# Kernel optimization log

Hardware: AMD Instinct MI355X
Metric: run time of the kernel (lower is better)

The kernel has to match this reference:

```python
import jax, jax.numpy as jnp
import numpy as np

FEA, ATT, HLAST, STEP = 256, 64, 10, 12
H = FEA * HLAST  # lstm hidden/cell size = 2560
IN = 2 * H       # concat(input, hidden) = 5120


def setup_inputs() -> dict:
    key = jax.random.key(0)
    ks = jax.random.split(key, 16)
    s = lambda k, shp, fan: jax.random.normal(k, shp, jnp.float32) * (1.0 / np.sqrt(fan))
    return {
        "x": jax.random.normal(ks[0], (64 * STEP, FEA, ATT), jnp.float32),
        # encoder: Linear(64->128), Linear(128->10) (stored as [in,out])
        "W0": s(ks[1], (ATT, 128), ATT), "b0": jnp.zeros((128,), jnp.float32),
        "W1": s(ks[2], (128, HLAST), 128), "b1": jnp.zeros((HLAST,), jnp.float32),
        # LSTM gates: forget, input, output, cell  [IN, H]
        "Wf": s(ks[3], (IN, H), IN), "bf": jnp.zeros((H,), jnp.float32),
        "Wi": s(ks[4], (IN, H), IN), "bi": jnp.zeros((H,), jnp.float32),
        "Wo": s(ks[5], (IN, H), IN), "bo": jnp.zeros((H,), jnp.float32),
        "Wc": s(ks[6], (IN, H), IN), "bc": jnp.zeros((H,), jnp.float32),
        # final fc: Linear(10->10)
        "Wfc": s(ks[7], (HLAST, HLAST), HLAST), "bfc": jnp.zeros((HLAST,), jnp.float32),
    }


def reference(x, W0, b0, W1, b1, Wf, bf, Wi, bi, Wo, bo, Wc, bc, Wfc, bfc):
    # encoder (dropout is identity at eval): Linear -> ReLU, twice
    h = x.reshape(-1, FEA, ATT)
    h = jax.nn.relu(h @ W0 + b0)            # [B*T, FEA, 128]
    h = jax.nn.relu(h @ W1 + b1)            # [B*T, FEA, 10]
    h = h.reshape(-1, STEP, H)              # [B, T, H]
    B = h.shape[0]

    def step_fn(carry, xt):
        hs, cs = carry                       # [B, H] each
        comb = jnp.concatenate([xt, hs], axis=1)  # [B, 2H]
        f = jax.nn.sigmoid(comb @ Wf + bf)
        i = jax.nn.sigmoid(comb @ Wi + bi)
        o = jax.nn.sigmoid(comb @ Wo + bo)
        g = jnp.tanh(comb @ Wc + bc)
        cs = f * cs + i * g
        hs = o * jnp.tanh(cs)
        return (hs, cs), None

    init = (jnp.zeros((B, H), h.dtype), jnp.zeros((B, H), h.dtype))
    (hs, _), _ = jax.lax.scan(step_fn, init, jnp.swapaxes(h, 0, 1))  # scan over time

    out = hs.reshape(B, FEA, HLAST)          # [B, 256, 10]
    out = jax.nn.relu(out) @ Wfc + bfc       # fc(ReLU(x))
    return out
```

## Files before the change

kernel.cpp:

```cpp
#include <hip/hip_runtime.h>
#include <math.h>

#define FEA   256
#define ATT   64
#define HLAST 10
#define NSTEP 12
#define HDIM  2560
#define BATCH 64
#define BT    768
#define KT_FULL 160
#define KT_HALF 80
#define NT_G  160
#define MT_E  48

typedef _Float16 h8_t __attribute__((ext_vector_type(8)));
typedef float    f4_t __attribute__((ext_vector_type(4)));

__device__ __forceinline__ float sigm(float x) { return 1.0f / (1.0f + expf(-x)); }

__global__ __launch_bounds__(256) void k_pack_enc(
    const float* __restrict__ W0, const float* __restrict__ W1,
    _Float16* __restrict__ Bp0, _Float16* __restrict__ Bp1)
{
  const int tid = threadIdx.x;
  for (int e = tid; e < 16 * 512; e += 256) {
    const int frag = e >> 9, idx = e & 511, l = idx >> 3, j = idx & 7;
    const int nt = frag >> 1, kt = frag & 1;
    const int k = kt * 32 + (l >> 4) * 8 + j;
    const int n = nt * 16 + (l & 15);
    Bp0[e] = (_Float16)W0[k * 128 + n];
  }
  for (int e = tid; e < 4 * 512; e += 256) {
    const int kt = e >> 9, idx = e & 511, l = idx >> 3, j = idx & 7;
    const int k = kt * 32 + (l >> 4) * 8 + j;
    const int n = l & 15;
    Bp1[e] = (n < HLAST) ? (_Float16)W1[k * HLAST + n] : (_Float16)0.0f;
  }
}

__global__ __launch_bounds__(256) void k_enc_conv(
    const float* __restrict__ x, const _Float16* __restrict__ Bp0,
    const _Float16* __restrict__ Bp1, const float* __restrict__ b0,
    const float* __restrict__ b1, _Float16* __restrict__ Ep,
    const float* __restrict__ Wf, const float* __restrict__ Wi,
    const float* __restrict__ Wo, const float* __restrict__ Wc,
    _Float16* __restrict__ Wp)
{
  __shared__ __align__(16) _Float16 sA[4][16][136];
  const int grp = blockIdx.x / 37, r37 = blockIdx.x % 37;
  const int tid = threadIdx.x;

  if (r37 >= 12) {
    float (*tile)[130] = (float(*)[130])(void*)sA;
    const int cid = grp * 25 + (r37 - 12);
    const int g = cid / 1600;
    const int r = cid % 1600;
    const int kt = r / 20, cb = r % 20;
    const float* __restrict__ W = (g == 0) ? Wf : (g == 1) ? Wi : (g == 2) ? Wo : Wc;
    const float* src = W + (size_t)(kt * 32) * HDIM + cb * 128;
    #pragma unroll
    for (int s = 0; s < 4; ++s) {
      const int slot = s * 256 + tid;
      const int rr = slot >> 5, c4 = slot & 31;
      float4 v = *(const float4*)&src[(size_t)rr * HDIM + c4 * 4];
      *(float4*)&tile[rr][c4 * 4] = v;
    }
    __syncthreads();
    const int l = tid & 63, w = tid >> 6;
    const int k0 = (l >> 4) * 8, c16 = l & 15;
    #pragma unroll
    for (int s = 0; s < 2; ++s) {
      const int f = w * 2 + s;
      h8_t h;
      #pragma unroll
      for (int j = 0; j < 8; ++j) h[j] = (_Float16)tile[k0 + j][f * 16 + c16];
      const int nt = cb * 8 + f;
      *(h8_t*)&Wp[(((size_t)(g * NT_G + nt) * KT_FULL + kt) << 9) + l * 8] = h;
    }
    return;
  }

  const int eid = grp * 12 + r37;
  const int l = tid & 63, w = tid >> 6;
  const int bt = eid >> 2;
  const int f0 = (eid & 3) * 64 + w * 16;
  const int rl = l >> 4, cl = l & 15;

  h8_t B0[16];
  #pragma unroll
  for (int q = 0; q < 16; ++q)
    B0[q] = *(const h8_t*)(Bp0 + (q << 9) + l * 8);

  const float* xr = x + ((size_t)bt * FEA + f0 + cl) * ATT + rl * 8;
  h8_t a0, a1;
  {
    float4 v0 = *(const float4*)(xr);
    float4 v1 = *(const float4*)(xr + 4);
    float4 v2 = *(const float4*)(xr + 32);
    float4 v3 = *(const float4*)(xr + 36);
    #pragma unroll
    for (int j = 0; j < 4; ++j) {
      a0[j]     = (_Float16)((const float*)&v0)[j];
      a0[4 + j] = (_Float16)((const float*)&v1)[j];
      a1[j]     = (_Float16)((const float*)&v2)[j];
      a1[4 + j] = (_Float16)((const float*)&v3)[j];
    }
  }
  f4_t acc1[8] = {};
  #pragma unroll
  for (int j = 0; j < 8; ++j) {
    acc1[j] = __builtin_amdgcn_mfma_f32_16x16x32_f16(a0, B0[j * 2 + 0], acc1[j], 0, 0, 0);
    acc1[j] = __builtin_amdgcn_mfma_f32_16x16x32_f16(a1, B0[j * 2 + 1], acc1[j], 0, 0, 0);
  }
  #pragma unroll
  for (int j = 0; j < 8; ++j) {
    const float bj = b0[j * 16 + cl];
    #pragma unroll
    for (int r = 0; r < 4; ++r)
      sA[w][rl * 4 + r][j * 16 + cl] = (_Float16)fmaxf(acc1[j][r] + bj, 0.0f);
  }
  f4_t acc2 = {};
  #pragma unroll
  for (int kt = 0; kt < 4; ++kt) {
    const h8_t a = *(const h8_t*)&sA[w][cl][kt * 32 + rl * 8];
    const h8_t b = *(const h8_t*)(Bp1 + (kt << 9) + l * 8);
    acc2 = __builtin_amdgcn_mfma_f32_16x16x32_f16(a, b, acc2, 0, 0, 0);
  }
  if (cl < HLAST) {
    const float b1v = b1[cl];
    #pragma unroll
    for (int r = 0; r < 4; ++r) {
      const int f = f0 + rl * 4 + r;
      const float val = fmaxf(acc2[r] + b1v, 0.0f);
      const int kf = f * HLAST + cl;
      const int mt = bt >> 4, kt2 = kf >> 5, gp = (kf >> 3) & 3, jj = kf & 7;
      Ep[(((size_t)mt * KT_HALF + kt2) << 9) + (((bt & 15) + 16 * gp) << 3) + jj] =
          (_Float16)val;
    }
  }
}

__global__ __launch_bounds__(512) void k_xpre_conv(
    const _Float16* __restrict__ Ep, _Float16* __restrict__ Wp,
    const float* __restrict__ bf, const float* __restrict__ bi,
    const float* __restrict__ bo, const float* __restrict__ bc,
    _Float16* __restrict__ Xpre,
    const float* __restrict__ Wf, const float* __restrict__ Wi,
    const float* __restrict__ Wo, const float* __restrict__ Wc)
{
  __shared__ __align__(16) _Float16 sB[2][16 * 512];
  const int bid = blockIdx.x, tid = threadIdx.x;

  if (bid % 21 != 0) {
    float (*tile)[130] = (float(*)[130])(void*)sB;
    const int cid = bid - bid / 21 - 1;
    const int g = cid / 1600;
    const int r = cid % 1600;
    const int kt = 80 + r / 20, cb = r % 20;
    const float* __restrict__ W = (g == 0) ? Wf : (g == 1) ? Wi : (g == 2) ? Wo : Wc;
    const float* src = W + (size_t)(kt * 32) * HDIM + cb * 128;
    #pragma unroll
    for (int s = 0; s < 2; ++s) {
      const int slot = s * 512 + tid;
      const int rr = slot >> 5, c4 = slot & 31;
      float4 v = *(const float4*)&src[(size_t)rr * HDIM + c4 * 4];
      *(float4*)&tile[rr][c4 * 4] = v;
    }
    __syncthreads();
    const int l = tid & 63, f = tid >> 6;
    const int k0 = (l >> 4) * 8, c16 = l & 15;
    h8_t h;
    #pragma unroll
    for (int j = 0; j < 8; ++j) h[j] = (_Float16)tile[k0 + j][f * 16 + c16];
    const int nt = cb * 8 + f;
    *(h8_t*)&Wp[(((size_t)(g * NT_G + nt) * KT_FULL + kt) << 9) + l * 8] = h;
    return;
  }

  const int rid = bid / 21;
  const int bx = rid % 40, by = (rid / 40) & 1, bz = rid / 80;
  const int g = bz, mh = by;
  const float* __restrict__ bias = (g == 0) ? bf : (g == 1) ? bi : (g == 2) ? bo : bc;
  const int nt0 = bx * 4;
  const int l = tid & 63, w = tid >> 6;
  const int mt0 = mh * 24 + w * 3;
  const _Float16* Bsrc = Wp + ((size_t)(g * NT_G + nt0) * KT_FULL) * 512 + l * 8;
  const _Float16* Asrc = Ep + ((size_t)mt0 * KT_HALF) * 512 + l * 8;

  f4_t acc[3][4] = {};

#define STAGE_XPRE(cc, buf)                                                       \
  {                                                                               \
    _Pragma("unroll")                                                             \
    for (int s = 0; s < 2; ++s) {                                                 \
      const int fi = s * 8 + w;                                                   \
      const int jj = fi >> 2, tt = fi & 3;                                        \
      const _Float16* gsrc = Bsrc + ((size_t)jj * KT_FULL + (cc) * 4 + tt) * 512; \
      __builtin_amdgcn_global_load_lds(                                           \
          (const __attribute__((address_space(1))) unsigned int*)(const void*)gsrc, \
          (__attribute__((address_space(3))) unsigned int*)(void*)&sB[buf][fi * 512], \
          16, 0, 0);                                                              \
    }                                                                             \
  }

  STAGE_XPRE(0, 0);
  __syncthreads();
  for (int cc = 0; cc < 20; ++cc) {
    const int buf = cc & 1;
    if (cc < 19) STAGE_XPRE(cc + 1, buf ^ 1);
    #pragma unroll
    for (int t = 0; t < 4; ++t) {
      const int kt = cc * 4 + t;
      h8_t b[4], a[3];
      #pragma unroll
      for (int j = 0; j < 4; ++j)
        b[j] = *(const h8_t*)&sB[buf][(j * 4 + t) * 512 + l * 8];
      #pragma unroll
      for (int i = 0; i < 3; ++i)
        a[i] = *(const h8_t*)(Asrc + ((size_t)i * KT_HALF + kt) * 512);
      #pragma unroll
      for (int i = 0; i < 3; ++i)
        #pragma unroll
        for (int j = 0; j < 4; ++j)
          acc[i][j] = __builtin_amdgcn_mfma_f32_16x16x32_f16(a[i], b[j], acc[i][j], 0, 0, 0);
    }
    __syncthreads();
  }

  const int rl = l >> 4, cl = l & 15;
  const int bn = nt0 * 16;
  #pragma unroll
  for (int j = 0; j < 4; ++j) {
    const int n = bn + j * 16 + cl;
    const float bv = bias[n];
    #pragma unroll
    for (int i = 0; i < 3; ++i)
      #pragma unroll
      for (int r = 0; r < 4; ++r) {
        const int m = (mt0 + i) * 16 + rl * 4 + r;
        Xpre[((size_t)g * BT + m) * HDIM + n] = (_Float16)(acc[i][j][r] + bv);
      }
  }
#undef STAGE_XPRE
}

__global__ __launch_bounds__(512) void k_step(
    const _Float16* __restrict__ hP, const _Float16* __restrict__ Wp,
    const _Float16* __restrict__ Xpre, float* __restrict__ cbuf,
    float* __restrict__ hbuf, _Float16* __restrict__ hPn, int tstep)
{
  __shared__ float pre_lds[8][32 * 17];
  const int tid = threadIdx.x, l = tid & 63, w = tid >> 6;
  const int g = w >> 1, kc = w & 1;
  const int nt = blockIdx.x, mh = blockIdx.y;
  const int kt0 = kc * 40;
  const int dir = tstep & 1;
  const int base = dir ? (kt0 + 39) : kt0;
  const int sgn = dir ? -1 : 1;

  const int ub = tid >> 4, un = tid & 15;
  const int brow = mh * 32 + ub;
  const int unf = nt * 16 + un;
  const size_t xr = ((size_t)brow * NSTEP + tstep) * HDIM + unf;
  const float xf = (float)Xpre[xr];
  const float xi = (float)Xpre[(size_t)1 * BT * HDIM + xr];
  const float xo = (float)Xpre[(size_t)2 * BT * HDIM + xr];
  const float xc = (float)Xpre[(size_t)3 * BT * HDIM + xr];
  const size_t ci = (size_t)brow * HDIM + unf;
  const float cold = cbuf[ci];

  const _Float16* Ab = hP + (((size_t)mh * 2 * KT_HALF) << 9) + l * 8;
  const _Float16* Bb = Wp + (((size_t)(g * NT_G + nt) * KT_FULL + KT_HALF) << 9) + l * 8;

  f4_t acc[2] = {};
  h8_t bq[12];
  #pragma unroll
  for (int s = 0; s < 12; ++s)
    bq[s] = *(const h8_t*)(Bb + ((size_t)(base + sgn * s) << 9));
  h8_t aq[4][2];
  #pragma unroll
  for (int s = 0; s < 4; ++s)
    #pragma unroll
    for (int i = 0; i < 2; ++i)
      aq[s][i] = *(const h8_t*)(Ab + (((size_t)(i * KT_HALF + base + sgn * s)) << 9));

  #pragma unroll
  for (int it = 0; it < 40; ++it) {
    const int kt = base + sgn * it;
    const h8_t bcur = bq[it % 12];
    const h8_t a0 = aq[it & 3][0], a1 = aq[it & 3][1];
    if (it < 28)
      bq[it % 12] = *(const h8_t*)(Bb + ((size_t)(kt + sgn * 12) << 9));
    if (it < 36) {
      aq[it & 3][0] = *(const h8_t*)(Ab + (((size_t)(0 * KT_HALF + kt + sgn * 4)) << 9));
      aq[it & 3][1] = *(const h8_t*)(Ab + (((size_t)(1 * KT_HALF + kt + sgn * 4)) << 9));
    }
    acc[0] = __builtin_amdgcn_mfma_f32_16x16x32_f16(a0, bcur, acc[0], 0, 0, 0);
    acc[1] = __builtin_amdgcn_mfma_f32_16x16x32_f16(a1, bcur, acc[1], 0, 0, 0);
  }

  float* pl = pre_lds[w];
  const int rl = l >> 4, cl = l & 15;
  #pragma unroll
  for (int i = 0; i < 2; ++i)
    #pragma unroll
    for (int r = 0; r < 4; ++r)
      pl[(i * 16 + rl * 4 + r) * 17 + cl] = acc[i][r];
  __syncthreads();
  {
    const int off = ub * 17 + un;
    float pf = xf, pi_ = xi, po = xo, pc = xc;
    #pragma unroll
    for (int kc2 = 0; kc2 < 2; ++kc2) {
      pf  += pre_lds[0 * 2 + kc2][off];
      pi_ += pre_lds[1 * 2 + kc2][off];
      po  += pre_lds[2 * 2 + kc2][off];
      pc  += pre_lds[3 * 2 + kc2][off];
    }
    const float f = sigm(pf), i_ = sigm(pi_), o = sigm(po), gg = tanhf(pc);
    const float cn = f * cold + i_ * gg;
    cbuf[ci] = cn;
    const float hn = o * tanhf(cn);
    if (tstep == NSTEP - 1) hbuf[ci] = hn;
    const int mt = brow >> 4, kt2 = unf >> 5, gp = (unf >> 3) & 3, j = unf & 7;
    hPn[(((size_t)mt * KT_HALF + kt2) << 9) + ((brow & 15) + 16 * gp) * 8 + j] = (_Float16)hn;
  }
}

__global__ __launch_bounds__(256) void k_out(
    const float* __restrict__ h, const float* __restrict__ Wfc,
    const float* __restrict__ bfc, float* __restrict__ out)
{
  __shared__ float sW[HLAST * HLAST], sb[HLAST];
  const int t = threadIdx.x;
  if (t < HLAST * HLAST) sW[t] = Wfc[t];
  if (t < HLAST) sb[t] = bfc[t];
  __syncthreads();
  const int idx = blockIdx.x * 256 + t;
  const int j = idx % HLAST;
  const int bf_ = idx / HLAST;
  float a = sb[j];
  #pragma unroll
  for (int k = 0; k < HLAST; ++k)
    a = fmaf(fmaxf(h[(size_t)bf_ * HLAST + k], 0.0f), sW[k * HLAST + j], a);
  out[idx] = a;
}

extern "C" void kernel_launch(void* const* d_in, const int* in_sizes, int n_in,
                              void* d_out, int out_size, void* d_ws, size_t ws_size,
                              hipStream_t stream)
{
  const float* x   = (const float*)d_in[0];
  const float* W0  = (const float*)d_in[1];
  const float* b0  = (const float*)d_in[2];
  const float* W1  = (const float*)d_in[3];
  const float* b1  = (const float*)d_in[4];
  const float* Wf  = (const float*)d_in[5];
  const float* bfp = (const float*)d_in[6];
  const float* Wi  = (const float*)d_in[7];
  const float* bip = (const float*)d_in[8];
  const float* Wo  = (const float*)d_in[9];
  const float* bop = (const float*)d_in[10];
  const float* Wc  = (const float*)d_in[11];
  const float* bcp = (const float*)d_in[12];
  const float* Wfc = (const float*)d_in[13];
  const float* bfc = (const float*)d_in[14];

  char* ws = (char*)d_ws;
  _Float16* Wp = (_Float16*)ws;                       ws += (size_t)4 * NT_G * KT_FULL * 512 * 2;
  _Float16* Ep = (_Float16*)ws;                       ws += (size_t)MT_E * KT_HALF * 512 * 2;
  _Float16* Xpre = (_Float16*)ws;                     ws += (size_t)4 * BT * HDIM * 2;
  float* cbuf  = (float*)ws;                          ws += (size_t)BATCH * HDIM * 4;
  float* hbuf  = (float*)ws;                          ws += (size_t)BATCH * HDIM * 4;
  _Float16* hPa = (_Float16*)ws;                      ws += (size_t)BATCH * HDIM * 2;
  _Float16* hPb = (_Float16*)ws;                      ws += (size_t)BATCH * HDIM * 2;
  _Float16* Bp0 = (_Float16*)ws;                      ws += (size_t)16 * 512 * 2;
  _Float16* Bp1 = (_Float16*)ws;                      ws += (size_t)4 * 512 * 2;

  hipMemsetAsync(cbuf, 0, (size_t)BATCH * HDIM * 4, stream);
  hipMemsetAsync(hPa, 0, (size_t)BATCH * HDIM * 2, stream);

  k_pack_enc<<<1, 256, 0, stream>>>(W0, W1, Bp0, Bp1);
  k_enc_conv<<<37 * 256, 256, 0, stream>>>(x, Bp0, Bp1, b0, b1, Ep,
                                           Wf, Wi, Wo, Wc, Wp);
  k_xpre_conv<<<21 * 320, 512, 0, stream>>>(Ep, Wp, bfp, bip, bop, bcp, Xpre,
                                            Wf, Wi, Wo, Wc);
  _Float16* hin = hPa;
  _Float16* hout = hPb;
  for (int t = 0; t < NSTEP; ++t) {
    k_step<<<dim3(NT_G, 2), 512, 0, stream>>>(hin, Wp, Xpre, cbuf, hbuf, hout, t);
    _Float16* tmp = hin; hin = hout; hout = tmp;
  }
  k_out<<<(BATCH * FEA * HLAST) / 256, 256, 0, stream>>>(hbuf, Wfc, bfc, (float*)d_out);
}
```

Measured before the change: 377.9 us.

## Merge batch halves into one block per column tile in LSTM step kernel

Each step-kernel block now covers all 64 batch rows instead of 32, so each loaded recurrent weight fragment feeds four MFMAs instead of two. This halves the reads of the large packed gate weights per step, at the cost of halving the grid to 160 blocks and doubling accumulator and LDS usage per block. The A-operand prefetch depth drops from 4 to 2 stages to keep register pressure in check.

```diff
diff --git a/kernel.cpp b/kernel.cpp
--- a/kernel.cpp
+++ b/kernel.cpp
@@ -249,81 +249,93 @@
     const _Float16* __restrict__ Xpre, float* __restrict__ cbuf,
     float* __restrict__ hbuf, _Float16* __restrict__ hPn, int tstep)
 {
-  __shared__ float pre_lds[8][32 * 17];
+  __shared__ float pre_lds[8][64 * 17];
   const int tid = threadIdx.x, l = tid & 63, w = tid >> 6;
   const int g = w >> 1, kc = w & 1;
-  const int nt = blockIdx.x, mh = blockIdx.y;
+  const int nt = blockIdx.x;
   const int kt0 = kc * 40;
   const int dir = tstep & 1;
   const int base = dir ? (kt0 + 39) : kt0;
   const int sgn = dir ? -1 : 1;
 
   const int ub = tid >> 4, un = tid & 15;
-  const int brow = mh * 32 + ub;
   const int unf = nt * 16 + un;
-  const size_t xr = ((size_t)brow * NSTEP + tstep) * HDIM + unf;
-  const float xf = (float)Xpre[xr];
-  const float xi = (float)Xpre[(size_t)1 * BT * HDIM + xr];
-  const float xo = (float)Xpre[(size_t)2 * BT * HDIM + xr];
-  const float xc = (float)Xpre[(size_t)3 * BT * HDIM + xr];
-  const size_t ci = (size_t)brow * HDIM + unf;
-  const float cold = cbuf[ci];
-
-  const _Float16* Ab = hP + (((size_t)mh * 2 * KT_HALF) << 9) + l * 8;
+  float xg0[4], xg1[4], cold0, cold1;
+  size_t ci0, ci1;
+  {
+    const size_t xr0 = ((size_t)ub * NSTEP + tstep) * HDIM + unf;
+    const size_t xr1 = ((size_t)(ub + 32) * NSTEP + tstep) * HDIM + unf;
+    #pragma unroll
+    for (int gg = 0; gg < 4; ++gg) {
+      xg0[gg] = (float)Xpre[(size_t)gg * BT * HDIM + xr0];
+      xg1[gg] = (float)Xpre[(size_t)gg * BT * HDIM + xr1];
+    }
+    ci0 = (size_t)ub * HDIM + unf;
+    ci1 = (size_t)(ub + 32) * HDIM + unf;
+    cold0 = cbuf[ci0];
+    cold1 = cbuf[ci1];
+  }
+
+  const _Float16* Ab = hP + l * 8;
   const _Float16* Bb = Wp + (((size_t)(g * NT_G + nt) * KT_FULL + KT_HALF) << 9) + l * 8;
 
-  f4_t acc[2] = {};
+  f4_t acc[4] = {};
   h8_t bq[12];
   #pragma unroll
   for (int s = 0; s < 12; ++s)
     bq[s] = *(const h8_t*)(Bb + ((size_t)(base + sgn * s) << 9));
-  h8_t aq[4][2];
-  #pragma unroll
-  for (int s = 0; s < 4; ++s)
-    #pragma unroll
-    for (int i = 0; i < 2; ++i)
+  h8_t aq[2][4];
+  #pragma unroll
+  for (int s = 0; s < 2; ++s)
+    #pragma unroll
+    for (int i = 0; i < 4; ++i)
       aq[s][i] = *(const h8_t*)(Ab + (((size_t)(i * KT_HALF + base + sgn * s)) << 9));
 
   #pragma unroll
   for (int it = 0; it < 40; ++it) {
     const int kt = base + sgn * it;
     const h8_t bcur = bq[it % 12];
-    const h8_t a0 = aq[it & 3][0], a1 = aq[it & 3][1];
+    const h8_t a0 = aq[it & 1][0], a1 = aq[it & 1][1];
+    const h8_t a2 = aq[it & 1][2], a3 = aq[it & 1][3];
     if (it < 28)
       bq[it % 12] = *(const h8_t*)(Bb + ((size_t)(kt + sgn * 12) << 9));
-    if (it < 36) {
-      aq[it & 3][0] = *(const h8_t*)(Ab + (((size_t)(0 * KT_HALF + kt + sgn * 4)) << 9));
-      aq[it & 3][1] = *(const h8_t*)(Ab + (((size_t)(1 * KT_HALF + kt + sgn * 4)) << 9));
+    if (it < 38) {
+      #pragma unroll
+      for (int i = 0; i < 4; ++i)
+        aq[it & 1][i] = *(const h8_t*)(Ab + (((size_t)(i * KT_HALF + kt + sgn * 2)) << 9));
     }
     acc[0] = __builtin_amdgcn_mfma_f32_16x16x32_f16(a0, bcur, acc[0], 0, 0, 0);
     acc[1] = __builtin_amdgcn_mfma_f32_16x16x32_f16(a1, bcur, acc[1], 0, 0, 0);
+    acc[2] = __builtin_amdgcn_mfma_f32_16x16x32_f16(a2, bcur, acc[2], 0, 0, 0);
+    acc[3] = __builtin_amdgcn_mfma_f32_16x16x32_f16(a3, bcur, acc[3], 0, 0, 0);
   }
 
   float* pl = pre_lds[w];
   const int rl = l >> 4, cl = l & 15;
   #pragma unroll
-  for (int i = 0; i < 2; ++i)
+  for (int i = 0; i < 4; ++i)
     #pragma unroll
     for (int r = 0; r < 4; ++r)
       pl[(i * 16 + rl * 4 + r) * 17 + cl] = acc[i][r];
   __syncthreads();
-  {
-    const int off = ub * 17 + un;
-    float pf = xf, pi_ = xi, po = xo, pc = xc;
-    #pragma unroll
-    for (int kc2 = 0; kc2 < 2; ++kc2) {
-      pf  += pre_lds[0 * 2 + kc2][off];
-      pi_ += pre_lds[1 * 2 + kc2][off];
-      po  += pre_lds[2 * 2 + kc2][off];
-      pc  += pre_lds[3 * 2 + kc2][off];
-    }
+  #pragma unroll
+  for (int h = 0; h < 2; ++h) {
+    const int row = ub + h * 32;
+    const int off = row * 17 + un;
+    const float* xg = h ? xg1 : xg0;
+    const float cold = h ? cold1 : cold0;
+    const size_t ci = h ? ci1 : ci0;
+    const float pf = xg[0] + pre_lds[0][off] + pre_lds[1][off];
+    const float pi_ = xg[1] + pre_lds[2][off] + pre_lds[3][off];
+    const float po = xg[2] + pre_lds[4][off] + pre_lds[5][off];
+    const float pc = xg[3] + pre_lds[6][off] + pre_lds[7][off];
     const float f = sigm(pf), i_ = sigm(pi_), o = sigm(po), gg = tanhf(pc);
     const float cn = f * cold + i_ * gg;
     cbuf[ci] = cn;
     const float hn = o * tanhf(cn);
     if (tstep == NSTEP - 1) hbuf[ci] = hn;
-    const int mt = brow >> 4, kt2 = unf >> 5, gp = (unf >> 3) & 3, j = unf & 7;
-    hPn[(((size_t)mt * KT_HALF + kt2) << 9) + ((brow & 15) + 16 * gp) * 8 + j] = (_Float16)hn;
+    const int mt = row >> 4, kt2 = unf >> 5, gp = (unf >> 3) & 3, j = unf & 7;
+    hPn[(((size_t)mt * KT_HALF + kt2) << 9) + ((row & 15) + 16 * gp) * 8 + j] = (_Float16)hn;
   }
 }
 
@@ -388,7 +400,7 @@
   _Float16* hin = hPa;
   _Float16* hout = hPb;
   for (int t = 0; t < NSTEP; ++t) {
-    k_step<<<dim3(NT_G, 2), 512, 0, stream>>>(hin, Wp, Xpre, cbuf, hbuf, hout, t);
+    k_step<<<NT_G, 512, 0, stream>>>(hin, Wp, Xpre, cbuf, hbuf, hout, t);
     _Float16* tmp = hin; hin = hout; hout = tmp;
   }
   k_out<<<(BATCH * FEA * HLAST) / 256, 256, 0, stream>>>(hbuf, Wfc, bfc, (float*)d_out);
```

Measured after the change: 439.2 us. 16.2% more time.
